# Performance work log

Measured on AMD Instinct MI355X. Metric: run time of the kernel, lower is better.

## Reference

```python
import jax, jax.numpy as jnp
import numpy as np

S, B, I, H, O = 4096, 64, 14, 256, 1


def _lstm_layer(xs, W_ih, W_hh, b_ih, b_hh, h, c):
    # Precompute input contribution for all timesteps in one big GEMM.
    # xs: [S, B, D_in] -> pre: [S, B, 4H]  (PyTorch gate order: i, f, g, o)
    pre = jnp.einsum('sbd,gd->sbg', xs, W_ih) + b_ih + b_hh

    def step(carry, px):
        h, c = carry
        gates = px + h @ W_hh.T  # [B, 4H]
        i, f, g, o = jnp.split(gates, 4, axis=-1)
        i = jax.nn.sigmoid(i)
        f = jax.nn.sigmoid(f)
        g = jnp.tanh(g)
        o = jax.nn.sigmoid(o)
        c = f * c + i * g
        h = o * jnp.tanh(c)
        return (h, c), h

    (_, _), hs = jax.lax.scan(step, (h, c), pre)
    return hs  # [S, B, H]


def setup_inputs() -> dict:
    key = jax.random.key(0)
    ks = jax.random.split(key, 14)
    s = 1.0 / np.sqrt(H)  # PyTorch LSTM init scale
    u = lambda k, shape: jax.random.uniform(k, shape, jnp.float32, -s, s)
    return {
        'x': jax.random.normal(ks[0], (S, B, I), jnp.float32),
        'h0': jax.random.normal(ks[1], (2, B, H), jnp.float32),
        'c0': jax.random.normal(ks[2], (2, B, H), jnp.float32),
        'W_ih0': u(ks[3], (4 * H, I)),
        'W_hh0': u(ks[4], (4 * H, H)),
        'b_ih0': u(ks[5], (4 * H,)),
        'b_hh0': u(ks[6], (4 * H,)),
        'W_ih1': u(ks[7], (4 * H, H)),
        'W_hh1': u(ks[8], (4 * H, H)),
        'b_ih1': u(ks[9], (4 * H,)),
        'b_hh1': u(ks[10], (4 * H,)),
        'W_fc': u(ks[11], (O, H)),
        'b_fc': u(ks[12], (O,)),
    }


def reference(x, h0, c0, W_ih0, W_hh0, b_ih0, b_hh0,
              W_ih1, W_hh1, b_ih1, b_hh1, W_fc, b_fc):
    hs0 = _lstm_layer(x, W_ih0, W_hh0, b_ih0, b_hh0, h0[0], c0[0])
    # dropout=0.4 between layers applies only in train mode; eval reference -> identity
    hs1 = _lstm_layer(hs0, W_ih1, W_hh1, b_ih1, b_hh1, h0[1], c0[1])
    out = jax.nn.relu(hs1)
    return out @ W_fc.T + b_fc  # [S, B, O]
```

## Files before the change

### kernel.cpp

```cpp
#include <hip/hip_runtime.h>


#define S_LEN 4096
#define BATCH 64
#define IN_DIM 14
#define HID 256
#define GATES 1024
#define K0 288
#define LDA0 296
#define K1 512
#define LDA1 520
#define GST 260

#define NFY(L, g, j, wv) ((((((L)*4 + (g)) * 4 + (j)) * 8) + (wv)) * 16)

typedef _Float16 half8 __attribute__((ext_vector_type(8)));
typedef float f32x4 __attribute__((ext_vector_type(4)));
typedef unsigned long long u64;
typedef unsigned int u32;

__device__ __forceinline__ float sigf(float z) { return 1.0f / (1.0f + __expf(-z)); }
__device__ __forceinline__ float tanhf2(float z) { return 2.0f / (1.0f + __expf(-2.0f * z)) - 1.0f; }

__device__ __forceinline__ u64 aload(const u64* p) {
    return __hip_atomic_load(p, __ATOMIC_RELAXED, __HIP_MEMORY_SCOPE_AGENT);
}
__device__ __forceinline__ void astore(u64* p, u64 v) {
    __hip_atomic_store(p, v, __ATOMIC_RELAXED, __HIP_MEMORY_SCOPE_AGENT);
}
__device__ __forceinline__ u32 aload32(const u32* p) {
    return __hip_atomic_load(p, __ATOMIC_RELAXED, __HIP_MEMORY_SCOPE_AGENT);
}
__device__ __forceinline__ void astore32(u32* p, u32 v) {
    __hip_atomic_store(p, v, __ATOMIC_RELAXED, __HIP_MEMORY_SCOPE_AGENT);
}
__device__ __forceinline__ u32 packh2(float a, float b) {
    union { _Float16 h[2]; u32 u; } q;
    q.h[0] = (_Float16)a; q.h[1] = (_Float16)b;
    return q.u;
}

__global__ void prep_weights(const float* __restrict__ Wih0, const float* __restrict__ Whh0,
                             const float* __restrict__ bih0, const float* __restrict__ bhh0,
                             const float* __restrict__ Wih1, const float* __restrict__ Whh1,
                             const float* __restrict__ bih1, const float* __restrict__ bhh1,
                             _Float16* __restrict__ wcat0, _Float16* __restrict__ wcat1,
                             float* __restrict__ b0, float* __restrict__ b1) {
    int idx0 = blockIdx.x * blockDim.x + threadIdx.x;
    int stride = gridDim.x * blockDim.x;
    for (int i = idx0; i < GATES * K0; i += stride) {
        int n = i / K0, k = i % K0;
        float v = 0.f;
        if (k < HID) v = Whh0[n * HID + k];
        else if (k < HID + IN_DIM) v = Wih0[n * IN_DIM + (k - HID)];
        wcat0[i] = (_Float16)v;
    }
    for (int i = idx0; i < GATES * K1; i += stride) {
        int n = i / K1, k = i % K1;
        float v = (k < HID) ? Whh1[n * HID + k] : Wih1[n * HID + (k - HID)];
        wcat1[i] = (_Float16)v;
    }
    for (int i = idx0; i < GATES; i += stride) {
        b0[i] = bih0[i] + bhh0[i];
        b1[i] = bih1[i] + bhh1[i];
    }
}

__global__ __launch_bounds__(512) void lstm_scan(
    const float* __restrict__ x, const float* __restrict__ h0g, const float* __restrict__ c0g,
    const _Float16* __restrict__ wcat0, const _Float16* __restrict__ wcat1,
    const float* __restrict__ b0, const float* __restrict__ b1,
    const float* __restrict__ wfc, const float* __restrict__ bfc,
    u64* __restrict__ h0ring, u64* __restrict__ h1ring,
    u32* __restrict__ nfy, u32* __restrict__ prog, float* __restrict__ out, int R0) {
    const int bi = blockIdx.x;
    const int x7 = bi & 7;
    const int g = x7 >> 1;
    const int sub = ((x7 & 1) << 2) | (bi >> 3);
    const int L = sub >> 2;
    const int j = sub & 3;

    const int tid = threadIdx.x;
    const int w = tid >> 6;
    const int lane = tid & 63;
    const int quad = lane >> 4;
    const int col = lane & 15;
    const int c0b = g * 16;
    const int pm = tid & 15;
    const int iu = tid >> 4;
    const int pu = iu * 2;
    const int gm = tid >> 5;
    const int gu = tid & 31;

    __shared__ __align__(16) _Float16 Ash[16 * LDA1];
    __shared__ float Gsh[16 * GST];
    __shared__ float WfS[HID];
    __shared__ u32 OwnH[512];

    u64* h0w = h0ring + (size_t)g * R0 * 2048;
    u64* h1w = h1ring + (size_t)g * 4 * 2048;
    const int R0m = R0 - 1;

    int peer[3];
    { int c = 0; for (int p = 0; p < 4; ++p) if (p != j) peer[c++] = p; }

    if (L == 0) {
        half8 wr[2][K0 / 32];
        float bs[2];
#pragma unroll
        for (int tt = 0; tt < 2; ++tt) {
            int t = w + 8 * tt;
            int n = (t >> 2) * 256 + j * 64 + (t & 3) * 16 + col;
            bs[tt] = b0[n];
            const _Float16* wp = wcat0 + (size_t)n * K0 + quad * 8;
#pragma unroll
            for (int kk = 0; kk < K0 / 32; ++kk) wr[tt][kk] = *(const half8*)(wp + kk * 32);
        }
        float cs0 = c0g[(size_t)(c0b + pm) * HID + j * 64 + pu];
        float cs1 = c0g[(size_t)(c0b + pm) * HID + j * 64 + pu + 1];
        {
            int m = tid >> 5, cw = tid & 31;
            const float* hp = h0g + (size_t)(c0b + m) * HID + cw * 8;
            half8 hv;
#pragma unroll
            for (int q2 = 0; q2 < 8; ++q2) hv[q2] = (_Float16)hp[q2];
            *(half8*)&Ash[m * LDA0 + cw * 8] = hv;
            if (cw >= IN_DIM) Ash[m * LDA0 + HID + cw] = (_Float16)0.f;
        }
        const int xm = tid / IN_DIM, xd = tid - xm * IN_DIM;
        if (tid < 16 * IN_DIM)
            Ash[xm * LDA0 + HID + xd] = (_Float16)x[(size_t)(c0b + xm) * IN_DIM + xd];
        __syncthreads();

        for (int s = 0; s < S_LEN; ++s) {
            float xpre = 0.f;
            if (tid < 16 * IN_DIM && s + 1 < S_LEN)
                xpre = x[((size_t)(s + 1) * BATCH + c0b + xm) * IN_DIM + xd];
            const u64* ap[3];
            u64 vv[3] = {0, 0, 0};
            if (s > 0) {
                const u64* base = h0w + (size_t)((s - 1) & R0m) * 2048;
#pragma unroll
                for (int i = 0; i < 3; ++i) { ap[i] = base + peer[i] * 512 + tid; vv[i] = aload(ap[i]); }
            }
            if (w == 0) {
                bool act = false; const u32* np = nullptr; int tgt = 0;
                if (lane < 24) {
                    act = (s > 0); np = nfy + NFY(0, g, peer[lane >> 3], lane & 7); tgt = s;
                } else if (lane < 28) {
                    act = ((s & 7) == 0) && (s + 2 > R0);
                    np = prog + g * 4 + (lane - 24); tgt = s + 2 - R0;
                }
                bool ok = !act;
                for (;;) {
                    if (!ok) ok = ((int)aload32(np) >= tgt);
                    if (__all(ok)) break;
                    __builtin_amdgcn_s_sleep(1);
                }
            }
            __syncthreads();
            if (s > 0) {
#pragma unroll
                for (int i = 0; i < 3; ++i) {
                    while ((u32)(vv[i] >> 32) != (u32)s) vv[i] = aload(ap[i]);
                    *(u32*)&Ash[gm * LDA0 + peer[i] * 64 + 2 * gu] = (u32)vv[i];
                }
            }
            __syncthreads();
            f32x4 acc0 = {bs[0], bs[0], bs[0], bs[0]};
            f32x4 acc1 = {bs[1], bs[1], bs[1], bs[1]};
#pragma unroll
            for (int kk = 0; kk < K0 / 32; ++kk) {
                half8 av = *(const half8*)&Ash[col * LDA0 + kk * 32 + quad * 8];
                acc0 = __builtin_amdgcn_mfma_f32_16x16x32_f16(av, wr[0][kk], acc0, 0, 0, 0);
                acc1 = __builtin_amdgcn_mfma_f32_16x16x32_f16(av, wr[1][kk], acc1, 0, 0, 0);
            }
#pragma unroll
            for (int r = 0; r < 4; ++r) {
                Gsh[(quad * 4 + r) * GST + w * 16 + col] = acc0[r];
                Gsh[(quad * 4 + r) * GST + (w + 8) * 16 + col] = acc1[r];
            }
            __syncthreads();
            {
                float iv = sigf(Gsh[pm * GST + pu]);
                float fv = sigf(Gsh[pm * GST + 64 + pu]);
                float gv = tanhf2(Gsh[pm * GST + 128 + pu]);
                float ov = sigf(Gsh[pm * GST + 192 + pu]);
                cs0 = fv * cs0 + iv * gv;
                float ha = ov * tanhf2(cs0);
                iv = sigf(Gsh[pm * GST + pu + 1]);
                fv = sigf(Gsh[pm * GST + 64 + pu + 1]);
                gv = tanhf2(Gsh[pm * GST + 128 + pu + 1]);
                ov = sigf(Gsh[pm * GST + 192 + pu + 1]);
                cs1 = fv * cs1 + iv * gv;
                float hb = ov * tanhf2(cs1);
                u32 hw = packh2(ha, hb);
                *(u32*)&Ash[pm * LDA0 + j * 64 + pu] = hw;
                astore(h0w + (size_t)(s & R0m) * 2048 + j * 512 + (pm * 32 + iu),
                       (u64)hw | ((u64)(u32)(s + 1) << 32));
            }
            asm volatile("s_waitcnt vmcnt(0)" ::: "memory");
            if (lane == 0) astore32(nfy + NFY(0, g, j, w), (u32)(s + 1));
            if (tid < 16 * IN_DIM && s + 1 < S_LEN)
                Ash[xm * LDA0 + HID + xd] = (_Float16)xpre;
            __syncthreads();
        }
    } else {
        half8 wr[2][K1 / 32];
        float bs[2];
#pragma unroll
        for (int tt = 0; tt < 2; ++tt) {
            int t = w + 8 * tt;
            int n = (t >> 2) * 256 + j * 64 + (t & 3) * 16 + col;
            bs[tt] = b1[n];
            const _Float16* wp = wcat1 + (size_t)n * K1 + quad * 8;
#pragma unroll
            for (int kk = 0; kk < K1 / 32; ++kk) wr[tt][kk] = *(const half8*)(wp + kk * 32);
        }
        for (int i = tid; i < HID; i += 512) WfS[i] = wfc[i];
        const float bfcv = bfc[0];
        float cs0 = c0g[(size_t)(BATCH + c0b + pm) * HID + j * 64 + pu];
        float cs1 = c0g[(size_t)(BATCH + c0b + pm) * HID + j * 64 + pu + 1];
        {
            int m = tid >> 5, cw = tid & 31;
            const float* hp = h0g + (size_t)(BATCH + c0b + m) * HID + cw * 8;
            half8 hv;
#pragma unroll
            for (int q2 = 0; q2 < 8; ++q2) hv[q2] = (_Float16)hp[q2];
            *(half8*)&Ash[m * LDA1 + cw * 8] = hv;
        }
        u32* progself = prog + g * 4 + j;
        const u64* hp0[4];
        u64 hv0[4];
#pragma unroll
        for (int p = 0; p < 4; ++p) { hp0[p] = h0w + p * 512 + tid; hv0[p] = aload(hp0[p]); }
        __syncthreads();

        for (int s = 0; s <= S_LEN; ++s) {
            const u64* ap[3];
            u64 vv[3] = {0, 0, 0};
            if (s > 0) {
                const u64* b1p = h1w + (size_t)((s - 1) & 3) * 2048;
#pragma unroll
                for (int i = 0; i < 3; ++i) { ap[i] = b1p + peer[i] * 512 + tid; vv[i] = aload(ap[i]); }
            }
            if (w == 0) {
                bool act = false; const u32* np = nullptr; int tgt = 0;
                if (lane < 24) {
                    act = (s > 0); np = nfy + NFY(1, g, peer[lane >> 3], lane & 7); tgt = s;
                } else if (lane < 56) {
                    int l2 = lane - 24;
                    act = (s < S_LEN); np = nfy + NFY(0, g, l2 >> 3, l2 & 7); tgt = s + 1;
                }
                bool ok = !act;
                for (;;) {
                    if (!ok) ok = ((int)aload32(np) >= tgt);
                    if (__all(ok)) break;
                    __builtin_amdgcn_s_sleep(1);
                }
            } else if (w == 7 && s >= 2) {
                int m = 4 * j + quad;
                float fa = 0.f;
#pragma unroll
                for (int k16 = 0; k16 < 16; ++k16) {
                    float hv = (float)Ash[m * LDA1 + col + 16 * k16];
                    fa += fmaxf(hv, 0.f) * WfS[col + 16 * k16];
                }
#pragma unroll
                for (int off = 1; off < 16; off <<= 1) fa += __shfl_xor(fa, off, 16);
                if (col == 0) out[(size_t)(s - 2) * BATCH + c0b + m] = fa + bfcv;
            }
            __syncthreads();
            if (s > 0) {
#pragma unroll
                for (int i = 0; i < 3; ++i) {
                    while ((u32)(vv[i] >> 32) != (u32)s) vv[i] = aload(ap[i]);
                    *(u32*)&Ash[gm * LDA1 + peer[i] * 64 + 2 * gu] = (u32)vv[i];
                }
                *(u32*)&Ash[gm * LDA1 + j * 64 + 2 * gu] = OwnH[tid];
            }
            if (s < S_LEN) {
#pragma unroll
                for (int p = 0; p < 4; ++p) {
                    while ((u32)(hv0[p] >> 32) != (u32)(s + 1)) hv0[p] = aload(hp0[p]);
                    *(u32*)&Ash[gm * LDA1 + HID + p * 64 + 2 * gu] = (u32)hv0[p];
                }
            }
            __syncthreads();
            if (s == S_LEN) {
                if (w == 7) {
                    int m = 4 * j + quad;
                    float fa = 0.f;
#pragma unroll
                    for (int k16 = 0; k16 < 16; ++k16) {
                        float hv = (float)Ash[m * LDA1 + col + 16 * k16];
                        fa += fmaxf(hv, 0.f) * WfS[col + 16 * k16];
                    }
#pragma unroll
                    for (int off = 1; off < 16; off <<= 1) fa += __shfl_xor(fa, off, 16);
                    if (col == 0) out[(size_t)(S_LEN - 1) * BATCH + c0b + m] = fa + bfcv;
                }
                break;
            }
            f32x4 acc0 = {bs[0], bs[0], bs[0], bs[0]};
            f32x4 acc1 = {bs[1], bs[1], bs[1], bs[1]};
#pragma unroll
            for (int kk = 0; kk < K1 / 32; ++kk) {
                half8 av = *(const half8*)&Ash[col * LDA1 + kk * 32 + quad * 8];
                acc0 = __builtin_amdgcn_mfma_f32_16x16x32_f16(av, wr[0][kk], acc0, 0, 0, 0);
                acc1 = __builtin_amdgcn_mfma_f32_16x16x32_f16(av, wr[1][kk], acc1, 0, 0, 0);
            }
#pragma unroll
            for (int r = 0; r < 4; ++r) {
                Gsh[(quad * 4 + r) * GST + w * 16 + col] = acc0[r];
                Gsh[(quad * 4 + r) * GST + (w + 8) * 16 + col] = acc1[r];
            }
            __syncthreads();
            {
                float iv = sigf(Gsh[pm * GST + pu]);
                float fv = sigf(Gsh[pm * GST + 64 + pu]);
                float gv = tanhf2(Gsh[pm * GST + 128 + pu]);
                float ov = sigf(Gsh[pm * GST + 192 + pu]);
                cs0 = fv * cs0 + iv * gv;
                float ha = ov * tanhf2(cs0);
                iv = sigf(Gsh[pm * GST + pu + 1]);
                fv = sigf(Gsh[pm * GST + 64 + pu + 1]);
                gv = tanhf2(Gsh[pm * GST + 128 + pu + 1]);
                ov = sigf(Gsh[pm * GST + 192 + pu + 1]);
                cs1 = fv * cs1 + iv * gv;
                float hb = ov * tanhf2(cs1);
                u32 hw = packh2(ha, hb);
                OwnH[pm * 32 + iu] = hw;
                astore(h1w + (size_t)(s & 3) * 2048 + j * 512 + (pm * 32 + iu),
                       (u64)hw | ((u64)(u32)(s + 1) << 32));
            }
            asm volatile("s_waitcnt vmcnt(0)" ::: "memory");
            if (lane == 0) astore32(nfy + NFY(1, g, j, w), (u32)(s + 1));
            if (s + 1 < S_LEN) {
#pragma unroll
                for (int p = 0; p < 4; ++p) {
                    hp0[p] = h0w + (size_t)((s + 1) & R0m) * 2048 + p * 512 + tid;
                    hv0[p] = aload(hp0[p]);
                }
            }
            if ((s & 7) == 7 && tid == 0) astore32(progself, (u32)(s + 1));
            __syncthreads();
        }
    }
}

extern "C" void kernel_launch(void* const* d_in, const int* in_sizes, int n_in,
                              void* d_out, int out_size, void* d_ws, size_t ws_size,
                              hipStream_t stream) {
    const float* x    = (const float*)d_in[0];
    const float* h0   = (const float*)d_in[1];
    const float* c0   = (const float*)d_in[2];
    const float* Wih0 = (const float*)d_in[3];
    const float* Whh0 = (const float*)d_in[4];
    const float* bih0 = (const float*)d_in[5];
    const float* bhh0 = (const float*)d_in[6];
    const float* Wih1 = (const float*)d_in[7];
    const float* Whh1 = (const float*)d_in[8];
    const float* bih1 = (const float*)d_in[9];
    const float* bhh1 = (const float*)d_in[10];
    const float* Wfc  = (const float*)d_in[11];
    const float* bfc  = (const float*)d_in[12];
    float* out = (float*)d_out;

    char* ws = (char*)d_ws;
    constexpr size_t OFF_WCAT0 = 0;
    constexpr size_t SZ_WCAT0 = (size_t)GATES * K0 * 2;
    constexpr size_t OFF_WCAT1 = OFF_WCAT0 + SZ_WCAT0;
    constexpr size_t SZ_WCAT1 = (size_t)GATES * K1 * 2;
    constexpr size_t OFF_B0 = OFF_WCAT1 + SZ_WCAT1;
    constexpr size_t OFF_B1 = OFF_B0 + 4096;
    constexpr size_t OFF_PROG = OFF_B1 + 4096;
    constexpr size_t SZ_PROG = 16384;
    constexpr size_t OFF_NFY = OFF_PROG + SZ_PROG;
    constexpr size_t SZ_NFY = 16384;
    constexpr size_t OFF_H1R = OFF_NFY + SZ_NFY;
    constexpr size_t SZ_H1R = (size_t)4 * 4 * 2048 * 8;
    constexpr size_t OFF_H0R = OFF_H1R + SZ_H1R;

    _Float16* wcat0 = (_Float16*)(ws + OFF_WCAT0);
    _Float16* wcat1 = (_Float16*)(ws + OFF_WCAT1);
    float* b0 = (float*)(ws + OFF_B0);
    float* b1 = (float*)(ws + OFF_B1);
    u32* prog = (u32*)(ws + OFF_PROG);
    u32* nfy = (u32*)(ws + OFF_NFY);
    u64* h1ring = (u64*)(ws + OFF_H1R);

    int R0 = 128;
    while (OFF_H0R + (size_t)4 * R0 * 2048 * 8 > ws_size && R0 > 16) R0 >>= 1;
    u64* h0ring = (u64*)(ws + OFF_H0R);

    hipMemsetAsync(prog, 0, SZ_PROG + SZ_NFY, stream);
    prep_weights<<<256, 256, 0, stream>>>(Wih0, Whh0, bih0, bhh0, Wih1, Whh1, bih1, bhh1,
                                          wcat0, wcat1, b0, b1);
    lstm_scan<<<32, 512, 0, stream>>>(x, h0, c0, wcat0, wcat1, b0, b1, Wfc, bfc,
                                      h0ring, h1ring, nfy, (u32*)prog, out, R0);
}
```

Baseline: 11.52 ms.

## Replace per-wave notify flags with tagged-data polling using cache-bypassing loads

```diff
diff --git a/kernel.cpp b/kernel.cpp
--- a/kernel.cpp
+++ b/kernel.cpp
@@ -12,8 +12,6 @@
 #define LDA1 520
 #define GST 260
 
-#define NFY(L, g, j, wv) ((((((L)*4 + (g)) * 4 + (j)) * 8) + (wv)) * 16)
-
 typedef _Float16 half8 __attribute__((ext_vector_type(8)));
 typedef float f32x4 __attribute__((ext_vector_type(4)));
 typedef unsigned long long u64;
@@ -22,22 +20,57 @@
 __device__ __forceinline__ float sigf(float z) { return 1.0f / (1.0f + __expf(-z)); }
 __device__ __forceinline__ float tanhf2(float z) { return 2.0f / (1.0f + __expf(-2.0f * z)) - 1.0f; }
 
-__device__ __forceinline__ u64 aload(const u64* p) {
-    return __hip_atomic_load(p, __ATOMIC_RELAXED, __HIP_MEMORY_SCOPE_AGENT);
-}
-__device__ __forceinline__ void astore(u64* p, u64 v) {
-    __hip_atomic_store(p, v, __ATOMIC_RELAXED, __HIP_MEMORY_SCOPE_AGENT);
-}
-__device__ __forceinline__ u32 aload32(const u32* p) {
-    return __hip_atomic_load(p, __ATOMIC_RELAXED, __HIP_MEMORY_SCOPE_AGENT);
-}
-__device__ __forceinline__ void astore32(u32* p, u32 v) {
-    __hip_atomic_store(p, v, __ATOMIC_RELAXED, __HIP_MEMORY_SCOPE_AGENT);
-}
 __device__ __forceinline__ u32 packh2(float a, float b) {
     union { _Float16 h[2]; u32 u; } q;
     q.h[0] = (_Float16)a; q.h[1] = (_Float16)b;
     return q.u;
+}
+
+__device__ __forceinline__ u64 ld64_c(const u64* p) {
+    u64 r;
+    asm volatile("global_load_dwordx2 %0, %1, off sc0 sc1\n\ts_waitcnt vmcnt(0)"
+                 : "=&v"(r) : "v"(p) : "memory");
+    return r;
+}
+__device__ __forceinline__ void st64_c(u64* p, u64 v) {
+    asm volatile("global_store_dwordx2 %0, %1, off sc0 sc1" :: "v"(p), "v"(v) : "memory");
+}
+__device__ __forceinline__ u32 ld32_c(const u32* p) {
+    u32 r;
+    asm volatile("global_load_dword %0, %1, off sc0 sc1\n\ts_waitcnt vmcnt(0)"
+                 : "=&v"(r) : "v"(p) : "memory");
+    return r;
+}
+__device__ __forceinline__ void st32_c(u32* p, u32 v) {
+    asm volatile("global_store_dword %0, %1, off sc0 sc1" :: "v"(p), "v"(v) : "memory");
+}
+__device__ __forceinline__ void ld64x3_c(const u64* p0, const u64* p1, const u64* p2,
+                                         u64& r0, u64& r1, u64& r2) {
+    asm volatile(
+        "global_load_dwordx2 %0, %3, off sc0 sc1\n\t"
+        "global_load_dwordx2 %1, %4, off sc0 sc1\n\t"
+        "global_load_dwordx2 %2, %5, off sc0 sc1\n\t"
+        "s_waitcnt vmcnt(0)"
+        : "=&v"(r0), "=&v"(r1), "=&v"(r2)
+        : "v"(p0), "v"(p1), "v"(p2)
+        : "memory");
+}
+__device__ __forceinline__ void ld64x7_c(
+    const u64* a0, const u64* a1, const u64* a2, const u64* a3,
+    const u64* p0, const u64* p1, const u64* p2,
+    u64& q0, u64& q1, u64& q2, u64& q3, u64& v0, u64& v1, u64& v2) {
+    asm volatile(
+        "global_load_dwordx2 %0, %7, off sc0 sc1\n\t"
+        "global_load_dwordx2 %1, %8, off sc0 sc1\n\t"
+        "global_load_dwordx2 %2, %9, off sc0 sc1\n\t"
+        "global_load_dwordx2 %3, %10, off sc0 sc1\n\t"
+        "global_load_dwordx2 %4, %11, off sc0 sc1\n\t"
+        "global_load_dwordx2 %5, %12, off sc0 sc1\n\t"
+        "global_load_dwordx2 %6, %13, off sc0 sc1\n\t"
+        "s_waitcnt vmcnt(0)"
+        : "=&v"(q0), "=&v"(q1), "=&v"(q2), "=&v"(q3), "=&v"(v0), "=&v"(v1), "=&v"(v2)
+        : "v"(a0), "v"(a1), "v"(a2), "v"(a3), "v"(p0), "v"(p1), "v"(p2)
+        : "memory");
 }
 
 __global__ void prep_weights(const float* __restrict__ Wih0, const float* __restrict__ Whh0,
@@ -72,7 +105,7 @@
     const float* __restrict__ b0, const float* __restrict__ b1,
     const float* __restrict__ wfc, const float* __restrict__ bfc,
     u64* __restrict__ h0ring, u64* __restrict__ h1ring,
-    u32* __restrict__ nfy, u32* __restrict__ prog, float* __restrict__ out, int R0) {
+    u32* __restrict__ prog, float* __restrict__ out, int R0) {
     const int bi = blockIdx.x;
     const int x7 = bi & 7;
     const int g = x7 >> 1;
@@ -104,6 +137,8 @@
     int peer[3];
     { int c = 0; for (int p = 0; p < 4; ++p) if (p != j) peer[c++] = p; }
 
+    int gbudget = 1 << 24;
+
     if (L == 0) {
         half8 wr[2][K0 / 32];
         float bs[2];
@@ -136,35 +171,25 @@
             float xpre = 0.f;
             if (tid < 16 * IN_DIM && s + 1 < S_LEN)
                 xpre = x[((size_t)(s + 1) * BATCH + c0b + xm) * IN_DIM + xd];
-            const u64* ap[3];
-            u64 vv[3] = {0, 0, 0};
+            if (w == 0 && lane < 4 && (s & 7) == 0 && s + 10 > R0) {
+                const u32* np = prog + g * 4 + lane;
+                int tgt = s + 10 - R0;
+                while ((int)ld32_c(np) < tgt && --gbudget > 0) __builtin_amdgcn_s_sleep(4);
+            }
             if (s > 0) {
                 const u64* base = h0w + (size_t)((s - 1) & R0m) * 2048;
-#pragma unroll
-                for (int i = 0; i < 3; ++i) { ap[i] = base + peer[i] * 512 + tid; vv[i] = aload(ap[i]); }
-            }
-            if (w == 0) {
-                bool act = false; const u32* np = nullptr; int tgt = 0;
-                if (lane < 24) {
-                    act = (s > 0); np = nfy + NFY(0, g, peer[lane >> 3], lane & 7); tgt = s;
-                } else if (lane < 28) {
-                    act = ((s & 7) == 0) && (s + 2 > R0);
-                    np = prog + g * 4 + (lane - 24); tgt = s + 2 - R0;
-                }
-                bool ok = !act;
-                for (;;) {
-                    if (!ok) ok = ((int)aload32(np) >= tgt);
-                    if (__all(ok)) break;
-                    __builtin_amdgcn_s_sleep(1);
-                }
-            }
-            __syncthreads();
-            if (s > 0) {
-#pragma unroll
-                for (int i = 0; i < 3; ++i) {
-                    while ((u32)(vv[i] >> 32) != (u32)s) vv[i] = aload(ap[i]);
-                    *(u32*)&Ash[gm * LDA0 + peer[i] * 64 + 2 * gu] = (u32)vv[i];
-                }
+                const u64* p0 = base + peer[0] * 512 + tid;
+                const u64* p1 = base + peer[1] * 512 + tid;
+                const u64* p2 = base + peer[2] * 512 + tid;
+                u64 v0, v1, v2;
+                ld64x3_c(p0, p1, p2, v0, v1, v2);
+                const u32 tg = (u32)s;
+                while ((u32)(v0 >> 32) != tg && --gbudget > 0) v0 = ld64_c(p0);
+                while ((u32)(v1 >> 32) != tg && --gbudget > 0) v1 = ld64_c(p1);
+                while ((u32)(v2 >> 32) != tg && --gbudget > 0) v2 = ld64_c(p2);
+                *(u32*)&Ash[gm * LDA0 + peer[0] * 64 + 2 * gu] = (u32)v0;
+                *(u32*)&Ash[gm * LDA0 + peer[1] * 64 + 2 * gu] = (u32)v1;
+                *(u32*)&Ash[gm * LDA0 + peer[2] * 64 + 2 * gu] = (u32)v2;
             }
             __syncthreads();
             f32x4 acc0 = {bs[0], bs[0], bs[0], bs[0]};
@@ -196,11 +221,9 @@
                 float hb = ov * tanhf2(cs1);
                 u32 hw = packh2(ha, hb);
                 *(u32*)&Ash[pm * LDA0 + j * 64 + pu] = hw;
-                astore(h0w + (size_t)(s & R0m) * 2048 + j * 512 + (pm * 32 + iu),
+                st64_c(h0w + (size_t)(s & R0m) * 2048 + j * 512 + (pm * 32 + iu),
                        (u64)hw | ((u64)(u32)(s + 1) << 32));
             }
-            asm volatile("s_waitcnt vmcnt(0)" ::: "memory");
-            if (lane == 0) astore32(nfy + NFY(0, g, j, w), (u32)(s + 1));
             if (tid < 16 * IN_DIM && s + 1 < S_LEN)
                 Ash[xm * LDA0 + HID + xd] = (_Float16)xpre;
             __syncthreads();
@@ -230,35 +253,10 @@
             *(half8*)&Ash[m * LDA1 + cw * 8] = hv;
         }
         u32* progself = prog + g * 4 + j;
-        const u64* hp0[4];
-        u64 hv0[4];
-#pragma unroll
-        for (int p = 0; p < 4; ++p) { hp0[p] = h0w + p * 512 + tid; hv0[p] = aload(hp0[p]); }
         __syncthreads();
 
         for (int s = 0; s <= S_LEN; ++s) {
-            const u64* ap[3];
-            u64 vv[3] = {0, 0, 0};
-            if (s > 0) {
-                const u64* b1p = h1w + (size_t)((s - 1) & 3) * 2048;
-#pragma unroll
-                for (int i = 0; i < 3; ++i) { ap[i] = b1p + peer[i] * 512 + tid; vv[i] = aload(ap[i]); }
-            }
-            if (w == 0) {
-                bool act = false; const u32* np = nullptr; int tgt = 0;
-                if (lane < 24) {
-                    act = (s > 0); np = nfy + NFY(1, g, peer[lane >> 3], lane & 7); tgt = s;
-                } else if (lane < 56) {
-                    int l2 = lane - 24;
-                    act = (s < S_LEN); np = nfy + NFY(0, g, l2 >> 3, l2 & 7); tgt = s + 1;
-                }
-                bool ok = !act;
-                for (;;) {
-                    if (!ok) ok = ((int)aload32(np) >= tgt);
-                    if (__all(ok)) break;
-                    __builtin_amdgcn_s_sleep(1);
-                }
-            } else if (w == 7 && s >= 2) {
+            if (w == 7 && s >= 2) {
                 int m = 4 * j + quad;
                 float fa = 0.f;
 #pragma unroll
@@ -270,21 +268,42 @@
                 for (int off = 1; off < 16; off <<= 1) fa += __shfl_xor(fa, off, 16);
                 if (col == 0) out[(size_t)(s - 2) * BATCH + c0b + m] = fa + bfcv;
             }
-            __syncthreads();
+            const u64* hb = h0w + (size_t)((s < S_LEN ? s : 0) & R0m) * 2048;
+            const u64* a0 = hb + tid;
+            const u64* a1 = hb + 512 + tid;
+            const u64* a2 = hb + 1024 + tid;
+            const u64* a3 = hb + 1536 + tid;
+            const u64* pb = h1w + (size_t)(((s > 0 ? s : 1) - 1) & 3) * 2048;
+            const u64* p0 = pb + peer[0] * 512 + tid;
+            const u64* p1 = pb + peer[1] * 512 + tid;
+            const u64* p2 = pb + peer[2] * 512 + tid;
+            u64 q0, q1, q2, q3, v0, v1, v2;
+            ld64x7_c(a0, a1, a2, a3, p0, p1, p2, q0, q1, q2, q3, v0, v1, v2);
+            if (s < S_LEN) {
+                const u32 tg = (u32)(s + 1);
+                while ((u32)(q0 >> 32) != tg && --gbudget > 0) q0 = ld64_c(a0);
+                while ((u32)(q1 >> 32) != tg && --gbudget > 0) q1 = ld64_c(a1);
+                while ((u32)(q2 >> 32) != tg && --gbudget > 0) q2 = ld64_c(a2);
+                while ((u32)(q3 >> 32) != tg && --gbudget > 0) q3 = ld64_c(a3);
+            }
             if (s > 0) {
-#pragma unroll
-                for (int i = 0; i < 3; ++i) {
-                    while ((u32)(vv[i] >> 32) != (u32)s) vv[i] = aload(ap[i]);
-                    *(u32*)&Ash[gm * LDA1 + peer[i] * 64 + 2 * gu] = (u32)vv[i];
-                }
+                const u32 tg = (u32)s;
+                while ((u32)(v0 >> 32) != tg && --gbudget > 0) v0 = ld64_c(p0);
+                while ((u32)(v1 >> 32) != tg && --gbudget > 0) v1 = ld64_c(p1);
+                while ((u32)(v2 >> 32) != tg && --gbudget > 0) v2 = ld64_c(p2);
+            }
+            __syncthreads();
+            if (s > 0) {
+                *(u32*)&Ash[gm * LDA1 + peer[0] * 64 + 2 * gu] = (u32)v0;
+                *(u32*)&Ash[gm * LDA1 + peer[1] * 64 + 2 * gu] = (u32)v1;
+                *(u32*)&Ash[gm * LDA1 + peer[2] * 64 + 2 * gu] = (u32)v2;
                 *(u32*)&Ash[gm * LDA1 + j * 64 + 2 * gu] = OwnH[tid];
             }
             if (s < S_LEN) {
-#pragma unroll
-                for (int p = 0; p < 4; ++p) {
-                    while ((u32)(hv0[p] >> 32) != (u32)(s + 1)) hv0[p] = aload(hp0[p]);
-                    *(u32*)&Ash[gm * LDA1 + HID + p * 64 + 2 * gu] = (u32)hv0[p];
-                }
+                *(u32*)&Ash[gm * LDA1 + HID + 0 * 64 + 2 * gu] = (u32)q0;
+                *(u32*)&Ash[gm * LDA1 + HID + 1 * 64 + 2 * gu] = (u32)q1;
+                *(u32*)&Ash[gm * LDA1 + HID + 2 * 64 + 2 * gu] = (u32)q2;
+                *(u32*)&Ash[gm * LDA1 + HID + 3 * 64 + 2 * gu] = (u32)q3;
             }
             __syncthreads();
             if (s == S_LEN) {
@@ -331,19 +350,10 @@
                 float hb = ov * tanhf2(cs1);
                 u32 hw = packh2(ha, hb);
                 OwnH[pm * 32 + iu] = hw;
-                astore(h1w + (size_t)(s & 3) * 2048 + j * 512 + (pm * 32 + iu),
+                st64_c(h1w + (size_t)(s & 3) * 2048 + j * 512 + (pm * 32 + iu),
                        (u64)hw | ((u64)(u32)(s + 1) << 32));
             }
-            asm volatile("s_waitcnt vmcnt(0)" ::: "memory");
-            if (lane == 0) astore32(nfy + NFY(1, g, j, w), (u32)(s + 1));
-            if (s + 1 < S_LEN) {
-#pragma unroll
-                for (int p = 0; p < 4; ++p) {
-                    hp0[p] = h0w + (size_t)((s + 1) & R0m) * 2048 + p * 512 + tid;
-                    hv0[p] = aload(hp0[p]);
-                }
-            }
-            if ((s & 7) == 7 && tid == 0) astore32(progself, (u32)(s + 1));
+            if ((s & 7) == 7 && tid == 0) st32_c(progself, (u32)(s + 1));
             __syncthreads();
         }
     }
@@ -375,10 +385,7 @@
     constexpr size_t OFF_B0 = OFF_WCAT1 + SZ_WCAT1;
     constexpr size_t OFF_B1 = OFF_B0 + 4096;
     constexpr size_t OFF_PROG = OFF_B1 + 4096;
-    constexpr size_t SZ_PROG = 16384;
-    constexpr size_t OFF_NFY = OFF_PROG + SZ_PROG;
-    constexpr size_t SZ_NFY = 16384;
-    constexpr size_t OFF_H1R = OFF_NFY + SZ_NFY;
+    constexpr size_t OFF_H1R = OFF_PROG + 4096;
     constexpr size_t SZ_H1R = (size_t)4 * 4 * 2048 * 8;
     constexpr size_t OFF_H0R = OFF_H1R + SZ_H1R;
 
@@ -387,16 +394,16 @@
     float* b0 = (float*)(ws + OFF_B0);
     float* b1 = (float*)(ws + OFF_B1);
     u32* prog = (u32*)(ws + OFF_PROG);
-    u32* nfy = (u32*)(ws + OFF_NFY);
     u64* h1ring = (u64*)(ws + OFF_H1R);
 
     int R0 = 128;
     while (OFF_H0R + (size_t)4 * R0 * 2048 * 8 > ws_size && R0 > 16) R0 >>= 1;
     u64* h0ring = (u64*)(ws + OFF_H0R);
 
-    hipMemsetAsync(prog, 0, SZ_PROG + SZ_NFY, stream);
+    hipMemsetAsync(ws + OFF_PROG, 0,
+                   (OFF_H0R - OFF_PROG) + (size_t)4 * R0 * 2048 * 8, stream);
     prep_weights<<<256, 256, 0, stream>>>(Wih0, Whh0, bih0, bhh0, Wih1, Whh1, bih1, bhh1,
                                           wcat0, wcat1, b0, b1);
     lstm_scan<<<32, 512, 0, stream>>>(x, h0, c0, wcat0, wcat1, b0, b1, Wfc, bfc,
-                                      h0ring, h1ring, nfy, (u32*)prog, out, R0);
-}
+                                      h0ring, h1ring, prog, out, R0);
+}
```

After: 10.74 ms. 6.8% less time.
